# Kernel tuning notes

Measured on AMD Instinct MI355X. Metric: run time of the kernel, lower is better.

The kernel has to match this reference:

```python
import jax, jax.numpy as jnp
import numpy as np
import math

B, S, D, H = 2, 1024, 4096, 32
HD = D // H  # 128
THETA = 500000.0


def setup_inputs() -> dict:
    key = jax.random.key(0)
    ks = jax.random.split(key, 6)
    x = jax.random.normal(ks[0], (B, S, D), dtype=jnp.float32)
    # RoPE frequencies (complex freqs_cis split into cos/sin), [S, HD//2]
    inv_freq = 1.0 / (THETA ** (jnp.arange(0, HD, 2, dtype=jnp.float32) / HD))
    angles = jnp.arange(S, dtype=jnp.float32)[:, None] * inv_freq[None, :]
    freqs_cos = jnp.cos(angles)
    freqs_sin = jnp.sin(angles)
    # Causal mask [1,1,S,S]: 0 on/below diag, large negative above
    neg = jnp.full((S, S), -1e9, dtype=jnp.float32)
    mask = jnp.triu(neg, k=1)[None, None]
    cache_k = jnp.zeros((B, S, H, HD), dtype=jnp.float32)
    cache_v = jnp.zeros((B, S, H, HD), dtype=jnp.float32)
    sc = 0.02
    wq = jax.random.normal(ks[1], (D, D), dtype=jnp.float32) * sc
    wk = jax.random.normal(ks[2], (D, D), dtype=jnp.float32) * sc
    wv = jax.random.normal(ks[3], (D, D), dtype=jnp.float32) * sc
    wo = jax.random.normal(ks[4], (D, D), dtype=jnp.float32) * sc
    return {"x": x, "freqs_cos": freqs_cos, "freqs_sin": freqs_sin,
            "mask": mask, "cache_k": cache_k, "cache_v": cache_v,
            "wq": wq, "wk": wk, "wv": wv, "wo": wo, "start_pos": 0}


def _apply_rope(t, cos, sin):
    # t: [B,S,H,HD]; cos/sin: [S,HD//2] -> complex multiply on (even, odd) pairs
    b, s, h, hd = t.shape
    tr = t.reshape(b, s, h, hd // 2, 2)
    te, to = tr[..., 0], tr[..., 1]
    c = cos[None, :, None, :]
    sn = sin[None, :, None, :]
    oe = te * c - to * sn
    oo = te * sn + to * c
    return jnp.stack([oe, oo], axis=-1).reshape(b, s, h, hd)


def reference(x, freqs_cos, freqs_sin, mask, cache_k, cache_v, wq, wk, wv, wo, start_pos):
    bsz, seqlen, dim = x.shape
    xq = (x @ wq.T).reshape(bsz, seqlen, H, HD)
    xk = (x @ wk.T).reshape(bsz, seqlen, H, HD)
    xv = (x @ wv.T).reshape(bsz, seqlen, H, HD)
    xq = _apply_rope(xq, freqs_cos, freqs_sin)
    xk = _apply_rope(xk, freqs_cos, freqs_sin)
    # KV-cache update
    cache_k = jax.lax.dynamic_update_slice(cache_k, xk, (0, start_pos, 0, 0))
    cache_v = jax.lax.dynamic_update_slice(cache_v, xv, (0, start_pos, 0, 0))
    keys = cache_k[:bsz, : start_pos + seqlen]    # [B,K,H,HD]
    values = cache_v[:bsz, : start_pos + seqlen]
    scores = jnp.einsum("bqhd,bkhd->bhqk", xq, keys) / math.sqrt(HD)
    scores = scores + mask
    probs = jax.nn.softmax(scores.astype(jnp.float32), axis=-1).astype(xq.dtype)
    out = jnp.einsum("bhqk,bkhd->bqhd", probs, values).reshape(bsz, seqlen, dim)
    return out @ wo.T
```

## Files before the change

### kernel.cpp

```cpp
#include <hip/hip_runtime.h>
#include <cstdint>
#include <cstddef>

typedef __bf16 bf16;
typedef bf16  bf16x8  __attribute__((ext_vector_type(8)));
typedef bf16  bf16x4  __attribute__((ext_vector_type(4)));
typedef float floatx4 __attribute__((ext_vector_type(4)));

#define D_MODEL 4096
#define NROWS   2048
#define SEQ     1024
#define NHEADS  32
#define HDIM    128

__device__ __forceinline__ void async16(const void* g, void* s) {
    __builtin_amdgcn_global_load_lds(
        (__attribute__((address_space(1))) void*)g,
        (__attribute__((address_space(3))) void*)s,
        16, 0, 0);
}

__global__ __launch_bounds__(256) void cvt_kernel(const float* __restrict__ in,
                                                  bf16* __restrict__ out, int n4) {
    int i = blockIdx.x * 256 + threadIdx.x;
    if (i >= n4) return;
    const float4 v = ((const float4*)in)[i];
    bf16x4 o;
    o[0] = (bf16)v.x; o[1] = (bf16)v.y; o[2] = (bf16)v.z; o[3] = (bf16)v.w;
    ((bf16x4*)out)[i] = o;
}

__global__ __launch_bounds__(256) void rope_kernel(bf16* __restrict__ Qb,
                                                   bf16* __restrict__ Kb,
                                                   const float* __restrict__ fc,
                                                   const float* __restrict__ fs) {
    int t = blockIdx.x * 256 + threadIdx.x;
    const bool isK = (t >> 20) != 0;
    bf16* p = isK ? Kb : Qb;
    const float qs = isK ? 1.0f : 0.08838834764831845f;
    int i = t & 1048575;
    int e = i * 8;
    int row = e >> 12;
    int coff = e & 4095;
    int s = row & 1023;
    int d0 = (coff & 127) >> 1;

    bf16x8 v = *(bf16x8*)(p + (size_t)row * D_MODEL + coff);
    float4 c4 = *(const float4*)&fc[s * 64 + d0];
    float4 s4 = *(const float4*)&fs[s * 64 + d0];
    float cc[4] = {c4.x, c4.y, c4.z, c4.w};
    float ss[4] = {s4.x, s4.y, s4.z, s4.w};
    bf16x8 o;
#pragma unroll
    for (int j = 0; j < 4; j++) {
        float e0 = (float)v[2 * j], e1 = (float)v[2 * j + 1];
        o[2 * j]     = (bf16)((e0 * cc[j] - e1 * ss[j]) * qs);
        o[2 * j + 1] = (bf16)((e0 * ss[j] + e1 * cc[j]) * qs);
    }
    *(bf16x8*)(p + (size_t)row * D_MODEL + coff) = o;
}

template<bool F32OUT>
__global__ __launch_bounds__(256) void gemm_bt(const bf16* __restrict__ A,
                                               const bf16* __restrict__ B0,
                                               void* __restrict__ C0) {
    __shared__ __align__(16) bf16 As[128 * 32];
    __shared__ __align__(16) bf16 Bs[128 * 32];
    const int tid  = threadIdx.x;
    const int lane = tid & 63;
    const int wave = tid >> 6;
    const int col  = lane & 15;
    const int quad = lane >> 4;
    const int bm = blockIdx.x * 128;
    const int bn = blockIdx.y * 128;
    const int wm = (wave >> 1) * 64;
    const int wn = (wave & 1) * 64;
    const bf16* Bw = B0 + (size_t)blockIdx.z * ((size_t)D_MODEL * D_MODEL);

    floatx4 acc[4][4] = {};

    for (int k0 = 0; k0 < D_MODEL; k0 += 32) {
#pragma unroll
        for (int j = 0; j < 2; j++) {
            int c   = j * 256 + tid;
            int row = c >> 2;
            int kc  = (c & 3) * 8;
            void* dstA = (void*)(As + (size_t)(j * 256 + wave * 64) * 8);
            void* dstB = (void*)(Bs + (size_t)(j * 256 + wave * 64) * 8);
            async16(A  + (size_t)(bm + row) * D_MODEL + k0 + kc, dstA);
            async16(Bw + (size_t)(bn + row) * D_MODEL + k0 + kc, dstB);
        }
        __syncthreads();
        bf16x8 a[4], b[4];
#pragma unroll
        for (int i = 0; i < 4; i++)
            a[i] = *(const bf16x8*)&As[(wm + i * 16 + col) * 32 + quad * 8];
#pragma unroll
        for (int j = 0; j < 4; j++)
            b[j] = *(const bf16x8*)&Bs[(wn + j * 16 + col) * 32 + quad * 8];
#pragma unroll
        for (int i = 0; i < 4; i++)
#pragma unroll
            for (int j = 0; j < 4; j++)
                acc[i][j] = __builtin_amdgcn_mfma_f32_16x16x32_bf16(a[i], b[j], acc[i][j], 0, 0, 0);
        __syncthreads();
    }

#pragma unroll
    for (int i = 0; i < 4; i++) {
#pragma unroll
        for (int j = 0; j < 4; j++) {
            int row = bm + wm + i * 16 + quad * 4;
            int cg  = bn + wn + j * 16 + col;
#pragma unroll
            for (int r = 0; r < 4; r++) {
                if constexpr (F32OUT) {
                    ((float*)C0)[(size_t)(row + r) * D_MODEL + cg] = acc[i][j][r];
                } else {
                    bf16* C = (bf16*)C0 + (size_t)blockIdx.z * ((size_t)NROWS * D_MODEL);
                    C[(size_t)(row + r) * D_MODEL + cg] = (bf16)acc[i][j][r];
                }
            }
        }
    }
}

#define PST 72

__global__ __launch_bounds__(256, 2) void attn_kernel(const bf16* __restrict__ Qb,
                                                      const bf16* __restrict__ Kb,
                                                      const bf16* __restrict__ Vb,
                                                      bf16* __restrict__ Ob) {
    __shared__ __align__(16) bf16 Ks[64 * 128];
    __shared__ __align__(16) bf16 Vt[128 * 64];
    __shared__ __align__(16) bf16 Ps[4 * 32 * PST];

    const int tid  = threadIdx.x;
    const int lane = tid & 63;
    const int wave = tid >> 6;
    const int col  = lane & 15;
    const int quad = lane >> 4;
    const int hb   = tid & 15;
    const int kb   = tid >> 4;

    const int b   = blockIdx.z;
    const int h   = blockIdx.y;
    const int ex  = b ? (7 - blockIdx.x) : blockIdx.x;
    const int q0b = ex * 128;
    const int q0w = q0b + wave * 32;
    const size_t bh = (size_t)(b * SEQ) * D_MODEL + h * HDIM;

    bf16x8 qf[2][4];
#pragma unroll
    for (int qi = 0; qi < 2; qi++)
#pragma unroll
        for (int kc = 0; kc < 4; kc++)
            qf[qi][kc] = *(const bf16x8*)(Qb + bh + (size_t)(q0w + qi * 16 + col) * D_MODEL + kc * 32 + quad * 8);

    floatx4 o[2][8];
    floatx4 ol[2];
#pragma unroll
    for (int qi = 0; qi < 2; qi++) {
        ol[qi] = (floatx4){0.f, 0.f, 0.f, 0.f};
#pragma unroll
        for (int c = 0; c < 8; c++) o[qi][c] = (floatx4){0.f, 0.f, 0.f, 0.f};
    }

    bf16x8 ones;
#pragma unroll
    for (int t = 0; t < 8; t++) ones[t] = (bf16)1.0f;

    bf16* Psw = Ps + wave * 32 * PST;
    const int nkt = ex * 2 + 2;

    for (int kt = 0; kt < nkt; kt++) {
        const int key0 = kt * 64;
#pragma unroll
        for (int it = 0; it < 4; it++) {
            int l = it * 256 + tid;
            int row = l >> 4, p = l & 15;
            int g = (p & 8) | ((p ^ (row & 7) ^ ((row >> 3) & 7)) & 7);
            async16(Kb + bh + (size_t)(key0 + row) * D_MODEL + g * 8,
                    (void*)(Ks + (size_t)(it * 256 + wave * 64) * 8));
        }
        {
            uint32_t uv[4][4];
#pragma unroll
            for (int i = 0; i < 4; i++) {
                uint4 t = *(const uint4*)(Vb + bh + (size_t)(key0 + kb * 4 + i) * D_MODEL + hb * 8);
                uv[i][0] = t.x; uv[i][1] = t.y; uv[i][2] = t.z; uv[i][3] = t.w;
            }
#pragma unroll
            for (int j = 0; j < 8; j++) {
                uint32_t sel = (j & 1) ? 0x07060302u : 0x05040100u;
                uint32_t w0 = __builtin_amdgcn_perm(uv[1][j >> 1], uv[0][j >> 1], sel);
                uint32_t w1 = __builtin_amdgcn_perm(uv[3][j >> 1], uv[2][j >> 1], sel);
                int row = hb * 8 + j;
                int p = ((kb >> 1) ^ (row & 7) ^ ((row >> 3) & 7)) & 7;
                uint2* dst = (uint2*)&Vt[row * 64 + p * 8 + (kb & 1) * 4];
                *dst = (uint2){w0, w1};
            }
        }
        __syncthreads();

        if (key0 <= q0w + 31) {
            const bool masked = (key0 + 63 > q0w);
            floatx4 sf[2][4];
#pragma unroll
            for (int qi = 0; qi < 2; qi++)
#pragma unroll
                for (int f = 0; f < 4; f++) sf[qi][f] = (floatx4){0.f, 0.f, 0.f, 0.f};
#pragma unroll
            for (int kc = 0; kc < 4; kc++)
#pragma unroll
                for (int f = 0; f < 4; f++) {
                    int row = f * 16 + col;
                    int g = kc * 4 + quad;
                    int p = (g & 8) | ((g ^ (row & 7) ^ ((row >> 3) & 7)) & 7);
                    bf16x8 kf = *(const bf16x8*)&Ks[row * 128 + p * 8];
                    sf[0][f] = __builtin_amdgcn_mfma_f32_16x16x32_bf16(qf[0][kc], kf, sf[0][f], 0, 0, 0);
                    sf[1][f] = __builtin_amdgcn_mfma_f32_16x16x32_bf16(qf[1][kc], kf, sf[1][f], 0, 0, 0);
                }
#pragma unroll
            for (int qi = 0; qi < 2; qi++)
#pragma unroll
                for (int f = 0; f < 4; f++) {
                    int key = key0 + f * 16 + col;
#pragma unroll
                    for (int r = 0; r < 4; r++) {
                        float pv;
                        if (masked)
                            pv = (key <= q0w + qi * 16 + quad * 4 + r) ? __expf(sf[qi][f][r]) : 0.f;
                        else
                            pv = __expf(sf[qi][f][r]);
                        Psw[(qi * 16 + quad * 4 + r) * PST + f * 16 + col] = (bf16)pv;
                    }
                }
#pragma unroll
            for (int kc = 0; kc < 2; kc++) {
                bf16x8 pa0 = *(const bf16x8*)&Psw[(0 * 16 + col) * PST + kc * 32 + quad * 8];
                bf16x8 pa1 = *(const bf16x8*)&Psw[(1 * 16 + col) * PST + kc * 32 + quad * 8];
                ol[0] = __builtin_amdgcn_mfma_f32_16x16x32_bf16(pa0, ones, ol[0], 0, 0, 0);
                ol[1] = __builtin_amdgcn_mfma_f32_16x16x32_bf16(pa1, ones, ol[1], 0, 0, 0);
#pragma unroll
                for (int c = 0; c < 8; c++) {
                    int row = c * 16 + col;
                    int g = kc * 4 + quad;
                    int p = (g ^ (row & 7) ^ ((row >> 3) & 7)) & 7;
                    bf16x8 vf = *(const bf16x8*)&Vt[row * 64 + p * 8];
                    o[0][c] = __builtin_amdgcn_mfma_f32_16x16x32_bf16(pa0, vf, o[0][c], 0, 0, 0);
                    o[1][c] = __builtin_amdgcn_mfma_f32_16x16x32_bf16(pa1, vf, o[1][c], 0, 0, 0);
                }
            }
        }
        __syncthreads();
    }

#pragma unroll
    for (int qi = 0; qi < 2; qi++) {
        float inv[4];
#pragma unroll
        for (int r = 0; r < 4; r++) inv[r] = 1.0f / ol[qi][r];
#pragma unroll
        for (int c = 0; c < 8; c++)
#pragma unroll
            for (int r = 0; r < 4; r++)
                Ob[bh + (size_t)(q0w + qi * 16 + quad * 4 + r) * D_MODEL + c * 16 + col] =
                    (bf16)(o[qi][c][r] * inv[r]);
    }
}

extern "C" void kernel_launch(void* const* d_in, const int* in_sizes, int n_in,
                              void* d_out, int out_size, void* d_ws, size_t ws_size,
                              hipStream_t stream) {
    const float* x  = (const float*)d_in[0];
    const float* fc = (const float*)d_in[1];
    const float* fs = (const float*)d_in[2];
    const float* wq = (const float*)d_in[6];
    const float* wk = (const float*)d_in[7];
    const float* wv = (const float*)d_in[8];
    const float* wo = (const float*)d_in[9];

    char* ws    = (char*)d_ws;
    bf16* xb    = (bf16*)(ws);
    bf16* wb    = (bf16*)(ws + 16777216ull);
    bf16* qkvb  = (bf16*)(ws + 117440512ull);
    bf16* attnb = (bf16*)(ws + 167772160ull);

    cvt_kernel<<<8192,  256, 0, stream>>>(x,  xb,                   2097152);
    cvt_kernel<<<16384, 256, 0, stream>>>(wq, wb + 0ull * 16777216, 4194304);
    cvt_kernel<<<16384, 256, 0, stream>>>(wk, wb + 1ull * 16777216, 4194304);
    cvt_kernel<<<16384, 256, 0, stream>>>(wv, wb + 2ull * 16777216, 4194304);

    gemm_bt<false><<<dim3(16, 32, 3), 256, 0, stream>>>(xb, wb, (void*)qkvb);

    cvt_kernel<<<16384, 256, 0, stream>>>(wo, wb, 4194304);

    rope_kernel<<<8192, 256, 0, stream>>>(qkvb, qkvb + 8388608ull, fc, fs);

    attn_kernel<<<dim3(8, 32, 2), 256, 0, stream>>>(qkvb, qkvb + 8388608ull,
                                                    qkvb + 16777216ull, attnb);

    gemm_bt<true><<<dim3(16, 32, 1), 256, 0, stream>>>(attnb, wb, d_out);
}
```

Before: 720.8 us.

## Replace QKV GEMM with 256x256-tile, 8-wave, multi-stage pipelined kernel

Adds a new fused QKV GEMM kernel that uses 256x256 output tiles with 8 waves per block and 8 LDS buffers filled by direct global-to-LDS async loads. The K loop is split into four phases that interleave the next stages' loads with MFMA work, using priority bumps and explicit vmcnt waits. It also remaps block IDs so tiles are grouped per XCD for L2 locality. The aim is to hide memory latency and improve operand reuse in the largest GEMM, at the cost of 128 KB of LDS per block, higher register pressure and fragile hand-managed pipelining.

```diff
diff --git a/kernel.cpp b/kernel.cpp
--- a/kernel.cpp
+++ b/kernel.cpp
@@ -125,6 +125,111 @@
     }
 }
 
+#define QSTAGE(buf, kh, ab, base, o0, o1, koff) do {                        \
+    bf16* s_ = &lds[(((buf) << 2) | ((kh) << 1) | (ab))][0];                \
+    async16((base) + (o0) + (koff), s_ + ldsw0);                            \
+    async16((base) + (o1) + (koff), s_ + 4096 + ldsw0);                     \
+} while (0)
+
+#define QPHASE(buf, kh, mh, STAGE_STMT, VM_STMT) do {                       \
+    const bf16* sA_ = &lds[(((buf) << 2) | ((kh) << 1))][0];                \
+    const bf16* sB_ = sA_ + 8192;                                           \
+    bf16x8 af_[4];                                                          \
+    _Pragma("unroll")                                                       \
+    for (int i_ = 0; i_ < 4; ++i_) {                                        \
+        int row_ = wm + ((mh) * 4 + i_) * 16 + col;                         \
+        af_[i_] = *(const bf16x8*)&sA_[row_ * 32 + quad * 8];               \
+    }                                                                       \
+    if ((mh) == 0) {                                                        \
+        _Pragma("unroll")                                                   \
+        for (int n_ = 0; n_ < 4; ++n_) {                                    \
+            int row_ = wn + n_ * 16 + col;                                  \
+            bfr[n_] = *(const bf16x8*)&sB_[row_ * 32 + quad * 8];           \
+        }                                                                   \
+    }                                                                       \
+    STAGE_STMT;                                                             \
+    __builtin_amdgcn_s_barrier();                                           \
+    __builtin_amdgcn_s_setprio(1);                                          \
+    _Pragma("unroll")                                                       \
+    for (int i_ = 0; i_ < 4; ++i_)                                          \
+        _Pragma("unroll")                                                   \
+        for (int n_ = 0; n_ < 4; ++n_)                                      \
+            acc[(mh) * 4 + i_][n_] = __builtin_amdgcn_mfma_f32_16x16x32_bf16( \
+                af_[i_], bfr[n_], acc[(mh) * 4 + i_][n_], 0, 0, 0);         \
+    __builtin_amdgcn_s_setprio(0);                                          \
+    VM_STMT;                                                                \
+    __builtin_amdgcn_s_barrier();                                           \
+} while (0)
+
+__global__ __launch_bounds__(512, 2) void gemm_qkv(const bf16* __restrict__ A,
+                                                   const bf16* __restrict__ W,
+                                                   bf16* __restrict__ C) {
+    __shared__ __align__(16) bf16 lds[8][8192];
+
+    const int tid  = threadIdx.x;
+    const int lane = tid & 63;
+    const int wave = tid >> 6;
+    const int col  = lane & 15;
+    const int quad = lane >> 4;
+
+    const int bid = blockIdx.x;
+    const int xcd = bid & 7;
+    const int li  = bid >> 3;
+    const int mt  = li & 7;
+    const int nt  = xcd * 6 + (li >> 3);
+    const int bm  = mt << 8;
+    const size_t bnr = (size_t)nt << 8;
+
+    const int wm = (wave >> 2) << 7;
+    const int wn = (wave & 3) << 6;
+
+    const int r0 = tid >> 2, g0 = tid & 3;
+    const size_t offA0 = (size_t)(bm + r0) * D_MODEL + g0 * 8;
+    const size_t offA1 = offA0 + (size_t)128 * D_MODEL;
+    const size_t offB0 = (bnr + (size_t)r0) * D_MODEL + g0 * 8;
+    const size_t offB1 = offB0 + (size_t)128 * D_MODEL;
+    const int ldsw0 = wave * 512;
+
+    floatx4 acc[8][4] = {};
+    bf16x8 bfr[4];
+
+    QSTAGE(0, 0, 0, A, offA0, offA1, 0);
+    QSTAGE(0, 0, 1, W, offB0, offB1, 0);
+    QSTAGE(0, 1, 0, A, offA0, offA1, 32);
+    QSTAGE(0, 1, 1, W, offB0, offB1, 32);
+    QSTAGE(1, 0, 1, W, offB0, offB1, 64);
+    QSTAGE(1, 0, 0, A, offA0, offA1, 64);
+    QSTAGE(1, 1, 1, W, offB0, offB1, 96);
+    asm volatile("s_waitcnt vmcnt(6)" ::: "memory");
+    __builtin_amdgcn_s_barrier();
+
+    for (int t = 0; t < 64; ++t) {
+        const int buf = t & 1;
+        const int k1 = ((t + 1 < 64) ? t + 1 : 63) * 64;
+        const int k2 = ((t + 2 < 64) ? t + 2 : 63) * 64;
+        QPHASE(buf, 0, 0, QSTAGE(buf ^ 1, 1, 0, A, offA0, offA1, k1 + 32), );
+        QPHASE(buf, 0, 1, QSTAGE(buf,     0, 1, W, offB0, offB1, k2), );
+        QPHASE(buf, 1, 0, QSTAGE(buf,     0, 0, A, offA0, offA1, k2), );
+        QPHASE(buf, 1, 1, QSTAGE(buf,     1, 1, W, offB0, offB1, k2 + 32),
+               asm volatile("s_waitcnt vmcnt(6)" ::: "memory"));
+    }
+    asm volatile("s_waitcnt vmcnt(0)" ::: "memory");
+
+    const size_t zb = (size_t)(nt >> 4) * ((size_t)NROWS * D_MODEL);
+    const int bn = (nt & 15) << 8;
+#pragma unroll
+    for (int m = 0; m < 8; ++m) {
+#pragma unroll
+        for (int n = 0; n < 4; ++n) {
+            const int row = bm + wm + m * 16 + quad * 4;
+            const int cg  = bn + wn + n * 16 + col;
+#pragma unroll
+            for (int r = 0; r < 4; ++r)
+                C[zb + (size_t)(row + r) * D_MODEL + cg] = (bf16)acc[m][n][r];
+        }
+    }
+}
+
 #define PST 72
 
 __global__ __launch_bounds__(256, 2) void attn_kernel(const bf16* __restrict__ Qb,
@@ -292,7 +397,7 @@
     cvt_kernel<<<16384, 256, 0, stream>>>(wk, wb + 1ull * 16777216, 4194304);
     cvt_kernel<<<16384, 256, 0, stream>>>(wv, wb + 2ull * 16777216, 4194304);
 
-    gemm_bt<false><<<dim3(16, 32, 3), 256, 0, stream>>>(xb, wb, (void*)qkvb);
+    gemm_qkv<<<dim3(384), 512, 0, stream>>>(xb, wb, qkvb);
 
     cvt_kernel<<<16384, 256, 0, stream>>>(wo, wb, 4194304);
 
```

Measured after the change: 731.9 us. No clear change (+1.5%).

## Replace GEMM with multi-stage pipelined 256x128 tile kernel and XCD-aware block mapping

Applied to the files above, without the earlier changes.

Replaces the single-buffered 128x128 GEMM with a 512-thread kernel that computes 256x128 tiles. It uses a four-slot LDS ring with async global-to-LDS prefetch two half-steps ahead, swizzled LDS addressing to avoid bank conflicts, and s_setprio around the MFMA bursts. Block IDs are remapped so each XCD works on a contiguous set of N tiles, which improves L2 reuse of the weights. The goal is to hide global load latency and cut barrier stalls, at the cost of more LDS per block and hand-tuned vmcnt waits that must stay consistent with the issue order.

```diff
diff --git a/kernel.cpp b/kernel.cpp
--- a/kernel.cpp
+++ b/kernel.cpp
@@ -60,65 +60,104 @@
     *(bf16x8*)(p + (size_t)row * D_MODEL + coff) = o;
 }
 
-template<bool F32OUT>
-__global__ __launch_bounds__(256) void gemm_bt(const bf16* __restrict__ A,
-                                               const bf16* __restrict__ B0,
-                                               void* __restrict__ C0) {
-    __shared__ __align__(16) bf16 As[128 * 32];
-    __shared__ __align__(16) bf16 Bs[128 * 32];
+#define ST2(sl, koff) do {                                                  \
+    bf16* da_ = &AS[(sl)][ldsw0];                                           \
+    async16(A + offA0 + (unsigned)(koff), da_);                             \
+    async16(A + offA1 + (unsigned)(koff), da_ + 4096);                      \
+    async16(W + offB0 + (unsigned)(koff), &BS[(sl)][ldsw0]);                \
+} while (0)
+
+#define PH2(sl, STAGE_STMT) do {                                            \
+    const bf16* sA_ = AS[(sl)];                                             \
+    const bf16* sB_ = BS[(sl)];                                             \
+    bf16x8 a_[4], b_[4];                                                    \
+    _Pragma("unroll")                                                       \
+    for (int m_ = 0; m_ < 4; ++m_) a_[m_] = *(const bf16x8*)&sA_[aoff + m_ * 512]; \
+    _Pragma("unroll")                                                       \
+    for (int n_ = 0; n_ < 4; ++n_) b_[n_] = *(const bf16x8*)&sB_[boff + n_ * 512]; \
+    STAGE_STMT;                                                             \
+    __builtin_amdgcn_s_barrier();                                           \
+    __builtin_amdgcn_s_setprio(1);                                          \
+    _Pragma("unroll")                                                       \
+    for (int m_ = 0; m_ < 4; ++m_)                                          \
+        _Pragma("unroll")                                                   \
+        for (int n_ = 0; n_ < 4; ++n_)                                      \
+            acc[m_][n_] = __builtin_amdgcn_mfma_f32_16x16x32_bf16(           \
+                a_[m_], b_[n_], acc[m_][n_], 0, 0, 0);                      \
+    __builtin_amdgcn_s_setprio(0);                                          \
+    asm volatile("s_waitcnt vmcnt(6)" ::: "memory");                        \
+    __builtin_amdgcn_s_barrier();                                           \
+} while (0)
+
+template<bool F32OUT, int NTPX>
+__global__ __launch_bounds__(512, 2) void gemm2(const bf16* __restrict__ A,
+                                                const bf16* __restrict__ W,
+                                                void* __restrict__ C0) {
+    __shared__ __align__(16) bf16 AS[4][8192];
+    __shared__ __align__(16) bf16 BS[4][4096];
+
     const int tid  = threadIdx.x;
     const int lane = tid & 63;
     const int wave = tid >> 6;
     const int col  = lane & 15;
     const int quad = lane >> 4;
-    const int bm = blockIdx.x * 128;
-    const int bn = blockIdx.y * 128;
-    const int wm = (wave >> 1) * 64;
-    const int wn = (wave & 1) * 64;
-    const bf16* Bw = B0 + (size_t)blockIdx.z * ((size_t)D_MODEL * D_MODEL);
+
+    const int bid = blockIdx.x;
+    const int xcd = bid & 7;
+    const int q   = bid >> 3;
+    const int sub = q >> 5;
+    const int gi  = q & 31;
+    const int mt  = gi & 7;
+    const int nt  = xcd * NTPX + sub * 4 + (gi >> 3);
+    const int bm  = mt << 8;
+
+    const int wm = (wave >> 1) << 6;
+    const int wn = (wave & 1) << 6;
+
+    const int dsw = ((tid & 7) - ((tid >> 3) & 7)) & 7;
+    const int ra  = ((tid >> 3) << 1) + (dsw >> 2);
+    const int ga  = dsw & 3;
+    const unsigned offA0 = (unsigned)(bm + ra) * D_MODEL + ga * 8;
+    const unsigned offA1 = offA0 + 128u * D_MODEL;
+    const unsigned offB0 = (unsigned)(nt * 128 + ra) * D_MODEL + ga * 8;
+    const int ldsw0 = wave * 512;
+
+    const int S    = (4 * (col & 1) + quad + (col >> 1)) & 7;
+    const int roff = (col >> 1) * 64 + S * 8;
+    const int aoff = (wm >> 1) * 64 + roff;
+    const int boff = (wn >> 1) * 64 + roff;
 
     floatx4 acc[4][4] = {};
 
-    for (int k0 = 0; k0 < D_MODEL; k0 += 32) {
-#pragma unroll
-        for (int j = 0; j < 2; j++) {
-            int c   = j * 256 + tid;
-            int row = c >> 2;
-            int kc  = (c & 3) * 8;
-            void* dstA = (void*)(As + (size_t)(j * 256 + wave * 64) * 8);
-            void* dstB = (void*)(Bs + (size_t)(j * 256 + wave * 64) * 8);
-            async16(A  + (size_t)(bm + row) * D_MODEL + k0 + kc, dstA);
-            async16(Bw + (size_t)(bn + row) * D_MODEL + k0 + kc, dstB);
-        }
-        __syncthreads();
-        bf16x8 a[4], b[4];
-#pragma unroll
-        for (int i = 0; i < 4; i++)
-            a[i] = *(const bf16x8*)&As[(wm + i * 16 + col) * 32 + quad * 8];
-#pragma unroll
-        for (int j = 0; j < 4; j++)
-            b[j] = *(const bf16x8*)&Bs[(wn + j * 16 + col) * 32 + quad * 8];
-#pragma unroll
-        for (int i = 0; i < 4; i++)
-#pragma unroll
-            for (int j = 0; j < 4; j++)
-                acc[i][j] = __builtin_amdgcn_mfma_f32_16x16x32_bf16(a[i], b[j], acc[i][j], 0, 0, 0);
-        __syncthreads();
-    }
-
-#pragma unroll
-    for (int i = 0; i < 4; i++) {
-#pragma unroll
-        for (int j = 0; j < 4; j++) {
-            int row = bm + wm + i * 16 + quad * 4;
-            int cg  = bn + wn + j * 16 + col;
-#pragma unroll
-            for (int r = 0; r < 4; r++) {
+    ST2(0, 0);
+    ST2(1, 32);
+    ST2(2, 64);
+    asm volatile("s_waitcnt vmcnt(6)" ::: "memory");
+    __builtin_amdgcn_s_barrier();
+
+    for (int t = 0; t < 64; ++t) {
+        const int buf = t & 1;
+        const int kA = ((t + 1 < 64) ? t + 1 : 63) * 64 + 32;
+        const int kB = ((t + 2 < 64) ? t + 2 : 63) * 64;
+        PH2(buf * 2 + 0, ST2((buf ^ 1) * 2 + 1, kA));
+        PH2(buf * 2 + 1, ST2(buf * 2 + 0, kB));
+    }
+    asm volatile("s_waitcnt vmcnt(0)" ::: "memory");
+
+    const int ncol = (nt & 31) << 7;
+#pragma unroll
+    for (int m = 0; m < 4; ++m) {
+#pragma unroll
+        for (int n = 0; n < 4; ++n) {
+            const int row = bm + wm + m * 16 + quad * 4;
+            const int cg  = ncol + wn + n * 16 + col;
+#pragma unroll
+            for (int r = 0; r < 4; ++r) {
                 if constexpr (F32OUT) {
-                    ((float*)C0)[(size_t)(row + r) * D_MODEL + cg] = acc[i][j][r];
+                    ((float*)C0)[(size_t)(row + r) * D_MODEL + cg] = acc[m][n][r];
                 } else {
-                    bf16* C = (bf16*)C0 + (size_t)blockIdx.z * ((size_t)NROWS * D_MODEL);
-                    C[(size_t)(row + r) * D_MODEL + cg] = (bf16)acc[i][j][r];
+                    bf16* C = (bf16*)C0 + (size_t)(nt >> 5) * ((size_t)NROWS * D_MODEL);
+                    C[(size_t)(row + r) * D_MODEL + cg] = (bf16)acc[m][n][r];
                 }
             }
         }
@@ -292,7 +331,7 @@
     cvt_kernel<<<16384, 256, 0, stream>>>(wk, wb + 1ull * 16777216, 4194304);
     cvt_kernel<<<16384, 256, 0, stream>>>(wv, wb + 2ull * 16777216, 4194304);
 
-    gemm_bt<false><<<dim3(16, 32, 3), 256, 0, stream>>>(xb, wb, (void*)qkvb);
+    gemm2<false, 12><<<dim3(768), 512, 0, stream>>>(xb, wb, (void*)qkvb);
 
     cvt_kernel<<<16384, 256, 0, stream>>>(wo, wb, 4194304);
 
@@ -301,5 +340,5 @@
     attn_kernel<<<dim3(8, 32, 2), 256, 0, stream>>>(qkvb, qkvb + 8388608ull,
                                                     qkvb + 16777216ull, attnb);
 
-    gemm_bt<true><<<dim3(16, 32, 1), 256, 0, stream>>>(attnb, wb, d_out);
-}
+    gemm2<true, 4><<<dim3(256), 512, 0, stream>>>(attnb, wb, d_out);
+}
```

Measured after the change: 749.7 us. 4.0% more time.
